# Performance work log

Hardware: AMD Instinct MI355X
Metric: run time of the kernel (lower is better)

Reference implementation:

```python
import jax, jax.numpy as jnp
import numpy as np

# dims
B, S, ENC, MARK = 8, 512, 7, 4
D, I, K, NH = 512, 1024, 4, 8          # embedding_dim, inner=2*D, conv kernel, heads
DH = I // NH                            # 128 per-head dim
BS_BLK = 4                              # qkv_proj_blocksize
NB = I // BS_BLK                        # 256 headwise blocks
L = 4                                   # num_blocks
PRED, COUT = 96, 7
EPS = 1e-6


def ln(x, w):
    mu = jnp.mean(x, -1, keepdims=True)
    var = jnp.var(x, -1, keepdims=True)
    return (x - mu) * jax.lax.rsqrt(var + 1e-5) * w


def causal_conv(x, w, b):
    # x [B,S,I], depthwise causal conv, kernel w [I,K]
    xp = jnp.pad(x, ((0, 0), (K - 1, 0), (0, 0)))
    kern = w.T[:, None, :]  # [K,1,I] for WIO with groups=I
    y = jax.lax.conv_general_dilated(xp, kern, (1,), 'VALID',
                                     dimension_numbers=('NWC', 'WIO', 'NWC'),
                                     feature_group_count=I)
    return y + b


def headwise(t, w):
    # block-diagonal linear (LinearHeadwiseExpand): t [B,S,I], w [NB,BS,BS]
    tb = t.reshape(B, S, NB, BS_BLK)
    return jnp.einsum('bsni,noi->bsno', tb, w).reshape(B, S, I)


def mlstm_parallel(q, k, v, ig, fg):
    # parallel_stabilized_simple: q,k,v [B,NH,S,DH]; ig,fg [B,NH,S]
    lf = jax.nn.log_sigmoid(fg)
    lfc = jnp.concatenate([jnp.zeros_like(lf[..., :1]), jnp.cumsum(lf, -1)], -1)  # [B,NH,S+1]
    m = (lfc[..., :, None] - lfc[..., None, :])[..., 1:, 1:]  # [B,NH,S,S]
    mask = jnp.tril(jnp.ones((S, S), dtype=bool))
    logD = jnp.where(mask, m + ig[..., None, :], -jnp.inf)
    maxD = jnp.max(logD, -1, keepdims=True)
    Dm = jnp.exp(logD - maxD)
    C = jnp.einsum('bnsd,bntd->bnst', q, k) * (DH ** -0.5) * Dm
    n = jnp.maximum(jnp.abs(jnp.sum(C, -1, keepdims=True)), jnp.exp(-maxD))
    return jnp.einsum('bnst,bntd->bnsd', C / (n + EPS), v)


def mh_norm(h, w):
    # per-head layernorm over DH, scale w [I]
    mu = jnp.mean(h, -1, keepdims=True)
    var = jnp.var(h, -1, keepdims=True)
    return (h - mu) * jax.lax.rsqrt(var + 1e-5) * w.reshape(1, NH, 1, DH)


def mlstm_block(x, p):
    lnw, upW, upb, cw, cb, wq, wk, wv, igW, igb, fgW, fgb, onw, skw, dW, db = p
    h = ln(x, lnw)                              # pre-norm
    u = h @ upW + upb                           # [B,S,2I]
    xm, z = jnp.split(u, 2, -1)
    xc = jax.nn.silu(causal_conv(xm, cw, cb))   # conv branch
    q = headwise(xc, wq)
    k = headwise(xc, wk)
    v = headwise(xm, wv)
    g = jnp.concatenate([q, k, v], -1)          # [B,S,3I]
    ig = (g @ igW + igb).transpose(0, 2, 1)     # [B,NH,S]
    fg = (g @ fgW + fgb).transpose(0, 2, 1)
    qh = q.reshape(B, S, NH, DH).transpose(0, 2, 1, 3)
    kh = k.reshape(B, S, NH, DH).transpose(0, 2, 1, 3)
    vh = v.reshape(B, S, NH, DH).transpose(0, 2, 1, 3)
    hh = mlstm_parallel(qh, kh, vh, ig, fg)
    hh = mh_norm(hh, onw).transpose(0, 2, 1, 3).reshape(B, S, I)
    hh = (hh + skw * xc) * jax.nn.silu(z)       # learnable skip + output gate
    return x + hh @ dW + db                     # residual


def setup_inputs() -> dict:
    key = jax.random.key(0)
    ks = jax.random.split(key, 16)
    r = lambda i, shape, s=0.02: jax.random.normal(ks[i], shape, jnp.float32) * s
    return {
        'x_enc': jax.random.normal(ks[0], (B, S, ENC), jnp.float32),
        'x_mark_enc': jax.random.normal(ks[1], (B, S, MARK), jnp.float32),
        'x_dec': jax.random.normal(ks[2], (B, PRED, ENC), jnp.float32),
        'x_mark_dec': jax.random.normal(ks[3], (B, PRED, MARK), jnp.float32),
        'emb_W': r(4, (ENC + MARK, D), 0.1), 'emb_b': jnp.zeros((D,), jnp.float32),
        'blk_ln_w': jnp.ones((L, D), jnp.float32),
        'up_W': r(5, (L, D, 2 * I)), 'up_b': jnp.zeros((L, 2 * I), jnp.float32),
        'conv_w': r(6, (L, I, K), 0.1), 'conv_b': jnp.zeros((L, I), jnp.float32),
        'Wq': r(7, (L, NB, BS_BLK, BS_BLK), 0.3),
        'Wk': r(8, (L, NB, BS_BLK, BS_BLK), 0.3),
        'Wv': r(9, (L, NB, BS_BLK, BS_BLK), 0.3),
        'ig_W': r(10, (L, 3 * I, NH), 0.01), 'ig_b': jnp.full((L, NH), -10.0, jnp.float32),
        'fg_W': r(11, (L, 3 * I, NH), 0.01),
        'fg_b': jnp.tile(jnp.linspace(3.0, 6.0, NH, dtype=jnp.float32)[None], (L, 1)),
        'onorm_w': jnp.ones((L, I), jnp.float32),
        'skip_w': jnp.ones((L, I), jnp.float32),
        'down_W': r(12, (L, I, D)), 'down_b': jnp.zeros((L, D), jnp.float32),
        'post_w': jnp.ones((D,), jnp.float32),
        'head_W': r(13, (D, COUT), 0.05), 'head_b': jnp.zeros((COUT,), jnp.float32),
    }


def reference(x_enc, x_mark_enc, x_dec, x_mark_dec, emb_W, emb_b, blk_ln_w,
              up_W, up_b, conv_w, conv_b, Wq, Wk, Wv, ig_W, ig_b, fg_W, fg_b,
              onorm_w, skip_w, down_W, down_b, post_w, head_W, head_b):
    x = jnp.concatenate([x_enc, x_mark_enc], -1) @ emb_W + emb_b  # [B,S,D]
    params = (blk_ln_w, up_W, up_b, conv_w, conv_b, Wq, Wk, Wv,
              ig_W, ig_b, fg_W, fg_b, onorm_w, skip_w, down_W, down_b)
    def step(c, p):
        return mlstm_block(c, p), None
    x, _ = jax.lax.scan(step, x, params)
    x = ln(x, post_w)                           # post_blocks_norm
    return x[:, -PRED:, :] @ head_W + head_b    # [B,PRED,COUT]
```

## Files before the change

kernel.cpp:

```cpp
#include <hip/hip_runtime.h>
#include <math.h>

static constexpr int kB = 8, kS = 512;
static constexpr int kD = 512, kI = 1024, kNH = 8, kDH = 128;
static constexpr int kL = 4, kPRED = 96, kCOUT = 7;
static constexpr int kM = kB * kS;

typedef __bf16 bf16x8 __attribute__((ext_vector_type(8)));
typedef float f32x4 __attribute__((ext_vector_type(4)));

#define MFMA_BF16(a, b, c) __builtin_amdgcn_mfma_f32_16x16x32_bf16((a), (b), (c), 0, 0, 0)

typedef __attribute__((address_space(1))) const unsigned char* as1cp;
typedef __attribute__((address_space(3))) unsigned char* as3p;
__device__ __forceinline__ void gload16(const void* g, void* l) {
  __builtin_amdgcn_global_load_lds((as1cp)g, (as3p)l, 16, 0, 0);
}

__device__ __forceinline__ unsigned short f2bf(float f) {
  union { float f; unsigned u; } v; v.f = f;
  unsigned r = v.u + 0x7fffu + ((v.u >> 16) & 1u);
  return (unsigned short)(r >> 16);
}
__device__ __forceinline__ float bf2f(unsigned short h) {
  union { unsigned u; float f; } v; v.u = (unsigned)h << 16; return v.f;
}

__global__ __launch_bounds__(256) void embed_ln_kernel(
    const float* __restrict__ xe, const float* __restrict__ xme,
    const float* __restrict__ W, const float* __restrict__ bias,
    const float* __restrict__ lnw,
    float* __restrict__ x, unsigned short* __restrict__ h) {
  int m = blockIdx.x;
  int tid = threadIdx.x;
  __shared__ float f[11];
  if (tid < 7) f[tid] = xe[m * 7 + tid];
  else if (tid < 11) f[tid] = xme[m * 4 + (tid - 7)];
  __syncthreads();
  float v0 = bias[tid], v1 = bias[256 + tid];
#pragma unroll
  for (int e = 0; e < 11; ++e) {
    v0 += f[e] * W[e * kD + tid];
    v1 += f[e] * W[e * kD + 256 + tid];
  }
  x[(size_t)m * kD + tid] = v0;
  x[(size_t)m * kD + 256 + tid] = v1;
  float s1 = v0 + v1, s2 = v0 * v0 + v1 * v1;
#pragma unroll
  for (int o = 1; o < 64; o <<= 1) { s1 += __shfl_xor(s1, o, 64); s2 += __shfl_xor(s2, o, 64); }
  __shared__ float a1[4], a2[4];
  if ((tid & 63) == 0) { a1[tid >> 6] = s1; a2[tid >> 6] = s2; }
  __syncthreads();
  float t1 = a1[0] + a1[1] + a1[2] + a1[3];
  float t2 = a2[0] + a2[1] + a2[2] + a2[3];
  float mu = t1 * (1.f / kD);
  float var = t2 * (1.f / kD) - mu * mu;
  float rs = rsqrtf(var + 1e-5f);
  h[(size_t)m * kD + tid] = f2bf((v0 - mu) * rs * lnw[tid]);
  h[(size_t)m * kD + 256 + tid] = f2bf((v1 - mu) * rs * lnw[256 + tid]);
}

__global__ __launch_bounds__(256) void ln_kernel(
    const float* __restrict__ x, const float* __restrict__ w, unsigned short* __restrict__ h) {
  int m = blockIdx.x, tid = threadIdx.x;
  float v0 = x[(size_t)m * kD + tid];
  float v1 = x[(size_t)m * kD + 256 + tid];
  float s1 = v0 + v1, s2 = v0 * v0 + v1 * v1;
#pragma unroll
  for (int o = 1; o < 64; o <<= 1) { s1 += __shfl_xor(s1, o, 64); s2 += __shfl_xor(s2, o, 64); }
  __shared__ float a1[4], a2[4];
  if ((tid & 63) == 0) { a1[tid >> 6] = s1; a2[tid >> 6] = s2; }
  __syncthreads();
  float t1 = a1[0] + a1[1] + a1[2] + a1[3];
  float t2 = a2[0] + a2[1] + a2[2] + a2[3];
  float mu = t1 * (1.f / kD);
  float var = t2 * (1.f / kD) - mu * mu;
  float rs = rsqrtf(var + 1e-5f);
  h[(size_t)m * kD + tid] = f2bf((v0 - mu) * rs * w[tid]);
  h[(size_t)m * kD + 256 + tid] = f2bf((v1 - mu) * rs * w[256 + tid]);
}

__global__ __launch_bounds__(256) void tpose_all_kernel(
    const float* __restrict__ upW, const float* __restrict__ dnW,
    const float* __restrict__ igW, const float* __restrict__ fgW,
    unsigned short* __restrict__ upWT, unsigned short* __restrict__ dnWT,
    unsigned short* __restrict__ gWT) {
  __shared__ float t[64][65];
  int id = blockIdx.x, tid = threadIdx.x;
  if (id < 1024) {
    int l = id >> 8, rem = id & 255;
    int n0 = (rem >> 3) * 64, k0 = (rem & 7) * 64;
    const float* Wl = upW + (size_t)l * 2048 * 512;
    unsigned short* WTl = upWT + (size_t)l * 2048 * 512;
    for (int idx = tid; idx < 4096; idx += 256) {
      int r = idx >> 6, c = idx & 63;
      t[r][c] = Wl[(size_t)(k0 + r) * 2048 + n0 + c];
    }
    __syncthreads();
    for (int idx = tid; idx < 4096; idx += 256) {
      int r = idx >> 6, c = idx & 63;
      WTl[(size_t)(n0 + r) * 512 + k0 + c] = f2bf(t[c][r]);
    }
  } else if (id < 1536) {
    int tt = id - 1024;
    int l = tt >> 7, rem = tt & 127;
    int n0 = (rem >> 4) * 64, k0 = (rem & 15) * 64;
    const float* Wl = dnW + (size_t)l * 512 * 1024;
    unsigned short* WTl = dnWT + (size_t)l * 512 * 1024;
    for (int idx = tid; idx < 4096; idx += 256) {
      int r = idx >> 6, c = idx & 63;
      t[r][c] = Wl[(size_t)(k0 + r) * 512 + n0 + c];
    }
    __syncthreads();
    for (int idx = tid; idx < 4096; idx += 256) {
      int r = idx >> 6, c = idx & 63;
      WTl[(size_t)(n0 + r) * 1024 + k0 + c] = f2bf(t[c][r]);
    }
  } else {
    int tt = id - 1536;
    int l = tt / 12, kc = tt % 12;
    int k = kc * 256 + tid;
    const float* igl = igW + (size_t)l * 3072 * 8;
    const float* fgl = fgW + (size_t)l * 3072 * 8;
    unsigned short* gl = gWT + (size_t)l * 16 * 3072;
#pragma unroll
    for (int h = 0; h < 8; ++h) {
      gl[(size_t)h * 3072 + k] = f2bf(igl[(size_t)k * 8 + h]);
      gl[(size_t)(8 + h) * 3072 + k] = f2bf(fgl[(size_t)k * 8 + h]);
    }
  }
}

template <int BM, int NBN, int RESID, typename TO>
__global__ __launch_bounds__(256) void gemm_mfma_kernel(
    const unsigned short* __restrict__ A, const unsigned short* __restrict__ BT,
    const float* __restrict__ bias, TO* __restrict__ C, int N, int Kd, int nwg) {
  constexpr int A_ISS = BM / 8;
  constexpr int PER_W = (A_ISS + 16) / 4;
  constexpr int MR = BM / 32;
  __shared__ __align__(16) char As[BM * 128];
  __shared__ __align__(16) char Bs[16384];
  int tid = threadIdx.x, w = tid >> 6, l = tid & 63;
  int lr = l & 15, lg = l >> 4;
  int id = blockIdx.x;
  int q = nwg >> 3, r = nwg & 7;
  int xcd = id & 7, pos = id >> 3;
  int wg = (xcd < r ? xcd * (q + 1) : r * (q + 1) + (xcd - r) * q) + pos;
  int bn = wg % NBN, bm = wg / NBN;
  int wrow = (w >> 1) * (BM / 2), wcol = (w & 1) * 64;
  f32x4 acc[MR][4] = {};
  for (int kt = 0; kt < Kd; kt += 64) {
    __syncthreads();
#pragma unroll
    for (int j = 0; j < PER_W; ++j) {
      int g = w * PER_W + j;
      bool isA = g < A_ISS;
      int ii = isA ? g : g - A_ISS;
      int row = ii * 8 + (l >> 3);
      int chunk = (l & 7) ^ (row & 7);
      const unsigned short* src = isA
          ? A + ((size_t)(bm * BM + row) * Kd + kt) + chunk * 8
          : BT + ((size_t)(bn * 128 + row) * Kd + kt) + chunk * 8;
      char* dst = (isA ? As : Bs) + ii * 1024;
      gload16(src, dst);
    }
    __syncthreads();
#pragma unroll
    for (int kk = 0; kk < 2; ++kk) {
      bf16x8 af[MR], bfr[4];
#pragma unroll
      for (int m = 0; m < MR; ++m) {
        int row = wrow + m * 16 + lr;
        int ch = (kk * 4 + lg) ^ (row & 7);
        af[m] = *(const bf16x8*)(As + row * 128 + ch * 16);
      }
#pragma unroll
      for (int n = 0; n < 4; ++n) {
        int row = wcol + n * 16 + lr;
        int ch = (kk * 4 + lg) ^ (row & 7);
        bfr[n] = *(const bf16x8*)(Bs + row * 128 + ch * 16);
      }
      __builtin_amdgcn_s_setprio(1);
#pragma unroll
      for (int m = 0; m < MR; ++m)
#pragma unroll
        for (int n = 0; n < 4; ++n)
          acc[m][n] = MFMA_BF16(af[m], bfr[n], acc[m][n]);
      __builtin_amdgcn_s_setprio(0);
    }
  }
#pragma unroll
  for (int n = 0; n < 4; ++n) {
    int col = bn * 128 + wcol + n * 16 + lr;
    float bv = bias[col];
#pragma unroll
    for (int m = 0; m < MR; ++m)
#pragma unroll
      for (int i = 0; i < 4; ++i) {
        int row = bm * BM + wrow + m * 16 + lg * 4 + i;
        float v = acc[m][n][i] + bv;
        if constexpr (sizeof(TO) == 2) {
          C[(size_t)row * N + col] = (TO)f2bf(v);
        } else {
          if (RESID) v += C[(size_t)row * N + col];
          C[(size_t)row * N + col] = v;
        }
      }
  }
}

__global__ __launch_bounds__(256) void convhead_kernel(
    const unsigned short* __restrict__ u, const float* __restrict__ cw,
    const float* __restrict__ cb,
    const float* __restrict__ Wq, const float* __restrict__ Wk, const float* __restrict__ Wv,
    unsigned short* __restrict__ xcb, unsigned short* __restrict__ qb,
    unsigned short* __restrict__ kb, unsigned short* __restrict__ vb) {
  int mb = blockIdx.x;
  int b = mb >> 7, sq = (mb & 127) * 4;
  int n = threadIdx.x;
  float xm[7][4];
#pragma unroll
  for (int j = 0; j < 7; ++j) {
    int sp = sq - 3 + j;
    if (sp >= 0) {
      unsigned long long raw = *(const unsigned long long*)&u[((size_t)(b * kS + sp)) * (2 * kI) + n * 4];
#pragma unroll
      for (int i = 0; i < 4; ++i) xm[j][i] = bf2f((unsigned short)(raw >> (i * 16)));
    } else {
#pragma unroll
      for (int i = 0; i < 4; ++i) xm[j][i] = 0.f;
    }
  }
  float4 cb4 = *(const float4*)&cb[n * 4];
  const float* cbp = &cb4.x;
  float cwv[4][4];
#pragma unroll
  for (int i = 0; i < 4; ++i) *(float4*)cwv[i] = *(const float4*)&cw[(n * 4 + i) * 4];
  float wqv[16], wkv[16], wvv[16];
#pragma unroll
  for (int o2 = 0; o2 < 4; ++o2) {
    *(float4*)&wqv[o2 * 4] = *(const float4*)&Wq[n * 16 + o2 * 4];
    *(float4*)&wkv[o2 * 4] = *(const float4*)&Wk[n * 16 + o2 * 4];
    *(float4*)&wvv[o2 * 4] = *(const float4*)&Wv[n * 16 + o2 * 4];
  }
#pragma unroll
  for (int t = 0; t < 4; ++t) {
    int s = sq + t;
    float xc[4];
    unsigned long long xcv = 0;
#pragma unroll
    for (int i = 0; i < 4; ++i) {
      float acc = cbp[i] + xm[t][i] * cwv[i][0] + xm[t + 1][i] * cwv[i][1] +
                  xm[t + 2][i] * cwv[i][2] + xm[t + 3][i] * cwv[i][3];
      xc[i] = acc / (1.f + __expf(-acc));
      xcv |= (unsigned long long)f2bf(xc[i]) << (i * 16);
    }
    *(unsigned long long*)&xcb[((size_t)(b * kS + s)) * kI + n * 4] = xcv;
    unsigned long long qv = 0, kv = 0, vv = 0;
#pragma unroll
    for (int o = 0; o < 4; ++o) {
      float aq = 0, ak = 0, av = 0;
#pragma unroll
      for (int i = 0; i < 4; ++i) {
        aq += xc[i] * wqv[o * 4 + i];
        ak += xc[i] * wkv[o * 4 + i];
        av += xm[t + 3][i] * wvv[o * 4 + i];
      }
      qv |= (unsigned long long)f2bf(aq) << (o * 16);
      kv |= (unsigned long long)f2bf(ak) << (o * 16);
      vv |= (unsigned long long)f2bf(av) << (o * 16);
    }
    size_t base = ((size_t)(b * 8 + (n >> 5)) * kS + s) * kDH + (n & 31) * 4;
    *(unsigned long long*)&qb[base] = qv;
    *(unsigned long long*)&kb[base] = kv;
    *(unsigned long long*)&vb[base] = vv;
  }
}

__global__ __launch_bounds__(256) void prep_kernel(
    const unsigned short* __restrict__ qb, const unsigned short* __restrict__ kb,
    const unsigned short* __restrict__ vb, const unsigned short* __restrict__ gWT,
    float* __restrict__ IGp, float* __restrict__ FGp, unsigned short* __restrict__ vt) {
  __shared__ __align__(16) char smem[16640];
  int id = blockIdx.x;
  int tid = threadIdx.x;
  if (id < 192) {
    int src = id >> 6;
    int blk = id & 63;
    int b = blk >> 3, s0 = (blk & 7) * 64;
    int w = tid >> 6, l = tid & 63;
    int lr = l & 15, lg = l >> 4;
    char* Ts = smem;
    const unsigned short* srcb = (src == 0) ? qb : (src == 1) ? kb : vb;
    f32x4 acc = {};
    for (int kc8 = 0; kc8 < 8; ++kc8) {
      const unsigned short* srcbase = srcb + ((size_t)(b * 8 + kc8) * kS + s0) * kDH;
      __syncthreads();
#pragma unroll
      for (int j = 0; j < 4; ++j) {
        int issue = w * 4 + j;
        int row = issue * 4 + (l >> 4);
        int chunk = (l & 15) ^ (row & 7);
        gload16(srcbase + row * 128 + chunk * 8, Ts + issue * 1024);
      }
      __syncthreads();
#pragma unroll
      for (int kk = 0; kk < 4; ++kk) {
        int arow = w * 16 + lr;
        int ch = (kk * 4 + lg) ^ (arow & 7);
        bf16x8 af = *(const bf16x8*)(Ts + arow * 256 + ch * 16);
        bf16x8 bfv = *(const bf16x8*)(gWT + (size_t)lr * 3072 + (src * 8 + kc8) * 128 + kk * 32 + lg * 8);
        acc = MFMA_BF16(af, bfv, acc);
      }
    }
    float* IGo = IGp + (size_t)src * 64 * kS;
    float* FGo = FGp + (size_t)src * 64 * kS;
#pragma unroll
    for (int i = 0; i < 4; ++i) {
      int s = s0 + w * 16 + lg * 4 + i;
      if (lr < 8) IGo[((size_t)(b * 8) + lr) * kS + s] = acc[i];
      else FGo[((size_t)(b * 8) + lr - 8) * kS + s] = acc[i];
    }
  } else {
    int t = id - 192;
    int bh = t >> 3, s0 = (t & 7) * 64;
    unsigned short (*tt)[130] = (unsigned short(*)[130])smem;
    for (int idx = tid; idx < 64 * 128; idx += 256) {
      int sl = idx >> 7, d = idx & 127;
      tt[sl][d] = vb[((size_t)bh * kS + s0 + sl) * kDH + d];
    }
    __syncthreads();
    for (int idx = tid; idx < 64 * 128; idx += 256) {
      int dl = idx >> 6, sl = idx & 63;
      vt[((size_t)bh * kDH + dl) * kS + s0 + sl] = tt[sl][dl];
    }
  }
}

__global__ __launch_bounds__(512) void mlstm_mfma_kernel(
    const unsigned short* __restrict__ qb, const unsigned short* __restrict__ kb,
    const unsigned short* __restrict__ vt,
    const float* __restrict__ IGp, const float* __restrict__ FGp,
    const float* __restrict__ igb, const float* __restrict__ fgb,
    const unsigned short* __restrict__ u, const unsigned short* __restrict__ xcb,
    const float* __restrict__ onw, const float* __restrict__ skw,
    unsigned short* __restrict__ hhb) {
  int id = blockIdx.x;
  int bh = (id & 7) * 8 + ((id >> 3) & 7);
  int pr = id >> 6;
  int rtA = 7 - pr, rtB = pr;
  int b = bh >> 3, nh = bh & 7;
  int tid = threadIdx.x, w = tid >> 6, l = tid & 63;
  int g = w >> 2, wl = w & 3;
  int rt = (g == 0) ? rtA : rtB;
  int lr = l & 15, lg = l >> 4;
  __shared__ __align__(16) char Ks[2][16384];
  __shared__ __align__(16) char Vs[2][16384];
  __shared__ __align__(16) char Ps[8][2048];
  __shared__ float avs[512], incs[512], pms[512];
  __shared__ float wsum[8], wmax[8];

  const unsigned short* kbh = kb + (size_t)bh * kS * kDH;
  const unsigned short* vbh = vt + (size_t)bh * kDH * kS;

#pragma unroll
  for (int j = 0; j < 2; ++j) {
    int issue = w * 2 + j;
    int row = issue * 4 + (l >> 4);
    int chunk = (l & 15) ^ (row & 7);
    gload16(kbh + row * 128 + chunk * 8, Ks[0] + issue * 1024);
  }
#pragma unroll
  for (int j = 0; j < 2; ++j) {
    int vi = w * 2 + j;
    int row = vi * 8 + (l >> 3);
    int chunk = (l & 7) ^ (row & 7);
    gload16(vbh + (size_t)row * kS + chunk * 8, Vs[0] + vi * 1024);
  }

  {
    int lane = tid & 63, wid2 = tid >> 6;
    const size_t ss = (size_t)64 * kS;
    size_t o = (size_t)bh * kS + tid;
    float igv = IGp[o] + IGp[ss + o] + IGp[2 * ss + o] + igb[nh];
    float fgv = FGp[o] + FGp[ss + o] + FGp[2 * ss + o] + fgb[nh];
    float lf = fminf(fgv, 0.f) - log1pf(__expf(-fabsf(fgv)));
    float x = lf;
#pragma unroll
    for (int off = 1; off < 64; off <<= 1) {
      float v = __shfl_up(x, off, 64);
      if (lane >= off) x += v;
    }
    if (lane == 63) wsum[wid2] = x;
    __syncthreads();
    float base = 0.f;
    for (int i2 = 0; i2 < wid2; ++i2) base += wsum[i2];
    float inct = x + base;
    incs[tid] = inct;
    float av = igv - inct;
    avs[tid] = 0.08838834764831845f * __expf(av);
    float y = av;
#pragma unroll
    for (int off = 1; off < 64; off <<= 1) {
      float v = __shfl_up(y, off, 64);
      if (lane >= off) y = fmaxf(y, v);
    }
    if (lane == 63) wmax[wid2] = y;
    __syncthreads();
    float mb2 = y;
    for (int i2 = 0; i2 < wid2; ++i2) mb2 = fmaxf(mb2, wmax[i2]);
    pms[tid] = mb2;
  }

  bf16x8 qf[4];
  int qrow = rt * 64 + wl * 16 + lr;
  const unsigned short* qrp = qb + ((size_t)bh * kS + qrow) * kDH + lg * 8;
#pragma unroll
  for (int kk = 0; kk < 4; ++kk) qf[kk] = *(const bf16x8*)(qrp + kk * 32);

  __syncthreads();

  float pm_r[4], epm[4];
#pragma unroll
  for (int i = 0; i < 4; ++i) {
    pm_r[i] = pms[rt * 64 + wl * 16 + lg * 4 + i];
    epm[i] = __expf(-pm_r[i]);
  }

  f32x4 oacc[8] = {};
  float rsum[4] = {};

  int cur = 0;
#pragma unroll 1
  for (int ct = 0; ct <= rtA; ++ct) {
    if (ct < rtA) {
      const unsigned short* kbase = kbh + (size_t)(ct + 1) * 64 * kDH;
      const unsigned short* vbase = vbh + (size_t)(ct + 1) * 64;
#pragma unroll
      for (int j = 0; j < 2; ++j) {
        int issue = w * 2 + j;
        int row = issue * 4 + (l >> 4);
        int chunk = (l & 15) ^ (row & 7);
        gload16(kbase + row * 128 + chunk * 8, Ks[cur ^ 1] + issue * 1024);
      }
#pragma unroll
      for (int j = 0; j < 2; ++j) {
        int vi = w * 2 + j;
        int row = vi * 8 + (l >> 3);
        int chunk = (l & 7) ^ (row & 7);
        gload16(vbase + (size_t)row * kS + chunk * 8, Vs[cur ^ 1] + vi * 1024);
      }
    }
    if (ct <= rt) {
      f32x4 sacc[4] = {};
      __builtin_amdgcn_s_setprio(1);
#pragma unroll
      for (int n = 0; n < 4; ++n) {
#pragma unroll
        for (int kk = 0; kk < 4; ++kk) {
          int krow = n * 16 + lr;
          int ch = (kk * 4 + lg) ^ (krow & 7);
          bf16x8 kf = *(const bf16x8*)(Ks[cur] + krow * 256 + ch * 16);
          sacc[n] = MFMA_BF16(qf[kk], kf, sacc[n]);
        }
      }
      __builtin_amdgcn_s_setprio(0);
#pragma unroll
      for (int n = 0; n < 4; ++n) {
        float eav = avs[ct * 64 + n * 16 + lr];
        int cg = ct * 64 + n * 16 + lr;
#pragma unroll
        for (int i = 0; i < 4; ++i) {
          int rg = rt * 64 + wl * 16 + lg * 4 + i;
          float s = 0.f;
          if (ct < rt || cg <= rg)
            s = sacc[n][i] * (eav * epm[i]);
          rsum[i] += s;
          int prow = lg * 4 + i, pcol = n * 16 + lr;
          int byte = prow * 128 + ((((pcol >> 3) ^ (prow & 7))) << 4) + (pcol & 7) * 2;
          *(unsigned short*)(Ps[w] + byte) = f2bf(s);
        }
      }
      __builtin_amdgcn_s_setprio(1);
#pragma unroll
      for (int kk = 0; kk < 2; ++kk) {
        int prow = lr;
        int pch = (kk * 4 + lg) ^ (prow & 7);
        bf16x8 pf = *(const bf16x8*)(Ps[w] + prow * 128 + pch * 16);
#pragma unroll
        for (int nb = 0; nb < 8; ++nb) {
          int vrow = nb * 16 + lr;
          int vch = (kk * 4 + lg) ^ (vrow & 7);
          bf16x8 vf = *(const bf16x8*)(Vs[cur] + vrow * 128 + vch * 16);
          oacc[nb] = MFMA_BF16(pf, vf, oacc[nb]);
        }
      }
      __builtin_amdgcn_s_setprio(0);
    }
    __syncthreads();
    cur ^= 1;
  }

#pragma unroll
  for (int i = 0; i < 4; ++i)
#pragma unroll
    for (int off = 1; off < 16; off <<= 1) rsum[i] += __shfl_xor(rsum[i], off, 16);
  float ninv[4];
#pragma unroll
  for (int i = 0; i < 4; ++i) {
    int rg = rt * 64 + wl * 16 + lg * 4 + i;
    float e0 = __expf(-incs[rg] - pm_r[i]);
    float nn = fmaxf(fabsf(rsum[i]), e0);
    ninv[i] = 1.f / (nn + 1e-6f);
  }
  float val[8][4];
  float s1[4] = {}, s2[4] = {};
#pragma unroll
  for (int nb = 0; nb < 8; ++nb)
#pragma unroll
    for (int i = 0; i < 4; ++i) {
      float v = oacc[nb][i] * ninv[i];
      val[nb][i] = v;
      s1[i] += v; s2[i] += v * v;
    }
#pragma unroll
  for (int i = 0; i < 4; ++i) {
#pragma unroll
    for (int off = 1; off < 16; off <<= 1) {
      s1[i] += __shfl_xor(s1[i], off, 16);
      s2[i] += __shfl_xor(s2[i], off, 16);
    }
  }
#pragma unroll
  for (int i = 0; i < 4; ++i) {
    int rg = rt * 64 + wl * 16 + lg * 4 + i;
    float mu = s1[i] * (1.f / 128.f);
    float var = s2[i] * (1.f / 128.f) - mu * mu;
    float rstd = rsqrtf(var + 1e-5f);
    size_t rowbase = (size_t)(b * kS + rg);
#pragma unroll
    for (int nb = 0; nb < 8; ++nb) {
      int c = nh * kDH + nb * 16 + lr;
      float nv = (val[nb][i] - mu) * rstd * onw[c];
      float z = bf2f(u[rowbase * (2 * kI) + kI + c]);
      float sz = z / (1.f + __expf(-z));
      float xcv = bf2f(xcb[rowbase * kI + c]);
      hhb[rowbase * kI + c] = f2bf((nv + skw[c] * xcv) * sz);
    }
  }
}

__global__ __launch_bounds__(256) void head_kernel(
    const float* __restrict__ x, const float* __restrict__ pw,
    const float* __restrict__ hW, const float* __restrict__ hb, float* __restrict__ out) {
  int row = blockIdx.x;
  int b = row / kPRED, p = row % kPRED;
  int m = b * kS + (kS - kPRED) + p;
  int tid = threadIdx.x;
  float v0 = x[(size_t)m * kD + tid];
  float v1 = x[(size_t)m * kD + 256 + tid];
  float s1 = v0 + v1, s2 = v0 * v0 + v1 * v1;
#pragma unroll
  for (int o = 1; o < 64; o <<= 1) { s1 += __shfl_xor(s1, o, 64); s2 += __shfl_xor(s2, o, 64); }
  __shared__ float a1[4], a2[4];
  if ((tid & 63) == 0) { a1[tid >> 6] = s1; a2[tid >> 6] = s2; }
  __syncthreads();
  float t1 = a1[0] + a1[1] + a1[2] + a1[3];
  float t2 = a2[0] + a2[1] + a2[2] + a2[3];
  float mu = t1 * (1.f / kD);
  float var = t2 * (1.f / kD) - mu * mu;
  float rs = rsqrtf(var + 1e-5f);
  __shared__ float buf[512];
  buf[tid] = (v0 - mu) * rs * pw[tid];
  buf[256 + tid] = (v1 - mu) * rs * pw[256 + tid];
  __syncthreads();
  float acc[7] = {};
  for (int kk = tid; kk < 512; kk += 256) {
    float g = buf[kk];
#pragma unroll
    for (int n = 0; n < 7; ++n) acc[n] += g * hW[kk * 7 + n];
  }
  __shared__ float red[256 * 9];
#pragma unroll
  for (int n = 0; n < 7; ++n) red[tid * 9 + n] = acc[n];
  __syncthreads();
  for (int off = 128; off >= 1; off >>= 1) {
    if (tid < off) {
#pragma unroll
      for (int n = 0; n < 7; ++n) red[tid * 9 + n] += red[(tid + off) * 9 + n];
    }
    __syncthreads();
  }
  if (tid < 7) out[(size_t)row * 7 + tid] = red[tid] + hb[tid];
}

extern "C" void kernel_launch(void* const* d_in, const int* in_sizes, int n_in,
                              void* d_out, int out_size, void* d_ws, size_t ws_size,
                              hipStream_t stream) {
  const float* x_enc    = (const float*)d_in[0];
  const float* x_mark   = (const float*)d_in[1];
  const float* emb_W    = (const float*)d_in[4];
  const float* emb_b    = (const float*)d_in[5];
  const float* blk_ln_w = (const float*)d_in[6];
  const float* up_W     = (const float*)d_in[7];
  const float* up_b     = (const float*)d_in[8];
  const float* conv_w   = (const float*)d_in[9];
  const float* conv_b   = (const float*)d_in[10];
  const float* Wq       = (const float*)d_in[11];
  const float* Wk       = (const float*)d_in[12];
  const float* Wv       = (const float*)d_in[13];
  const float* ig_W     = (const float*)d_in[14];
  const float* ig_b     = (const float*)d_in[15];
  const float* fg_W     = (const float*)d_in[16];
  const float* fg_b     = (const float*)d_in[17];
  const float* onorm_w  = (const float*)d_in[18];
  const float* skip_w   = (const float*)d_in[19];
  const float* down_W   = (const float*)d_in[20];
  const float* down_b   = (const float*)d_in[21];
  const float* post_w   = (const float*)d_in[22];
  const float* head_W   = (const float*)d_in[23];
  const float* head_b   = (const float*)d_in[24];
  float* out = (float*)d_out;

  char* ws = (char*)d_ws;
  float* X  = (float*)ws;                     ws += (size_t)kM * kD * 4;
  unsigned short* U    = (unsigned short*)ws; ws += (size_t)kM * 2 * kI * 2;
  unsigned short* XCb  = (unsigned short*)ws; ws += (size_t)kM * kI * 2;
  unsigned short* Hb   = (unsigned short*)ws; ws += (size_t)kM * kD * 2;
  unsigned short* HHb  = (unsigned short*)ws; ws += (size_t)kM * kI * 2;
  unsigned short* qb   = (unsigned short*)ws; ws += (size_t)kM * kI * 2;
  unsigned short* kbuf = (unsigned short*)ws; ws += (size_t)kM * kI * 2;
  unsigned short* vb   = (unsigned short*)ws; ws += (size_t)kM * kI * 2;
  unsigned short* vt   = (unsigned short*)ws; ws += (size_t)kM * kI * 2;
  unsigned short* upWT = (unsigned short*)ws; ws += (size_t)kL * 2 * kI * kD * 2;
  unsigned short* dnWT = (unsigned short*)ws; ws += (size_t)kL * kD * kI * 2;
  unsigned short* gWT  = (unsigned short*)ws; ws += (size_t)kL * 16 * 3072 * 2;
  float* IGp = (float*)ws; ws += (size_t)3 * 64 * kS * 4;
  float* FGp = (float*)ws; ws += (size_t)3 * 64 * kS * 4;

  embed_ln_kernel<<<kM, 256, 0, stream>>>(x_enc, x_mark, emb_W, emb_b, blk_ln_w, X, Hb);
  tpose_all_kernel<<<1584, 256, 0, stream>>>(up_W, down_W, ig_W, fg_W, upWT, dnWT, gWT);

  for (int l = 0; l < kL; ++l) {
    const float* lnw  = blk_ln_w + (size_t)l * kD;
    const float* upbl = up_b + (size_t)l * 2 * kI;
    const float* cwl  = conv_w + (size_t)l * kI * 4;
    const float* cbl  = conv_b + (size_t)l * kI;
    const float* wql  = Wq + (size_t)l * 256 * 16;
    const float* wkl  = Wk + (size_t)l * 256 * 16;
    const float* wvl  = Wv + (size_t)l * 256 * 16;
    const float* igbl = ig_b + (size_t)l * kNH;
    const float* fgbl = fg_b + (size_t)l * kNH;
    const float* onwl = onorm_w + (size_t)l * kI;
    const float* skwl = skip_w + (size_t)l * kI;
    const float* dbl  = down_b + (size_t)l * kD;
    const unsigned short* upWTl = upWT + (size_t)l * 2 * kI * kD;
    const unsigned short* dnWTl = dnWT + (size_t)l * kD * kI;
    const unsigned short* gWTl  = gWT + (size_t)l * 16 * 3072;

    if (l > 0) ln_kernel<<<kM, 256, 0, stream>>>(X, lnw, Hb);
    gemm_mfma_kernel<128, 16, 0, unsigned short><<<512, 256, 0, stream>>>(
        Hb, upWTl, upbl, U, 2 * kI, kD, 512);
    convhead_kernel<<<1024, 256, 0, stream>>>(U, cwl, cbl, wql, wkl, wvl, XCb, qb, kbuf, vb);
    prep_kernel<<<704, 256, 0, stream>>>(qb, kbuf, vb, gWTl, IGp, FGp, vt);
    mlstm_mfma_kernel<<<256, 512, 0, stream>>>(
        qb, kbuf, vt, IGp, FGp, igbl, fgbl, U, XCb, onwl, skwl, HHb);
    gemm_mfma_kernel<64, 4, 1, float><<<256, 256, 0, stream>>>(
        HHb, dnWTl, dbl, X, kD, kI, 256);
  }

  head_kernel<<<kB * kPRED, 256, 0, stream>>>(X, post_w, head_W, head_b, out);
}
```

Baseline: 388.4 us.

## Fold block LayerNorm into up-projection GEMM epilogue via row stats and colsums

Removes the per-layer LayerNorm kernel. The down-projection GEMM epilogue now writes a bf16 copy of the residual stream plus partial per-row sum and sum-of-squares. The up GEMM multiplies raw bf16 x by weights pre-scaled with the LN weight, then applies mean and rstd correction using precomputed weight column sums. The embedding, transpose and colsum setup are merged into one init kernel. This saves a launch and a memory pass per layer. The cost is extra epilogue work, and the numerics differ because normalization happens after bf16 quantization of the un-centered x, with possible cancellation error.

```diff
diff --git a/kernel.cpp b/kernel.cpp
--- a/kernel.cpp
+++ b/kernel.cpp
@@ -26,71 +26,52 @@
   union { unsigned u; float f; } v; v.u = (unsigned)h << 16; return v.f;
 }
 
-__global__ __launch_bounds__(256) void embed_ln_kernel(
+__global__ __launch_bounds__(256) void init_kernel(
     const float* __restrict__ xe, const float* __restrict__ xme,
-    const float* __restrict__ W, const float* __restrict__ bias,
-    const float* __restrict__ lnw,
-    float* __restrict__ x, unsigned short* __restrict__ h) {
-  int m = blockIdx.x;
-  int tid = threadIdx.x;
-  __shared__ float f[11];
-  if (tid < 7) f[tid] = xe[m * 7 + tid];
-  else if (tid < 11) f[tid] = xme[m * 4 + (tid - 7)];
-  __syncthreads();
-  float v0 = bias[tid], v1 = bias[256 + tid];
-#pragma unroll
-  for (int e = 0; e < 11; ++e) {
-    v0 += f[e] * W[e * kD + tid];
-    v1 += f[e] * W[e * kD + 256 + tid];
-  }
-  x[(size_t)m * kD + tid] = v0;
-  x[(size_t)m * kD + 256 + tid] = v1;
-  float s1 = v0 + v1, s2 = v0 * v0 + v1 * v1;
-#pragma unroll
-  for (int o = 1; o < 64; o <<= 1) { s1 += __shfl_xor(s1, o, 64); s2 += __shfl_xor(s2, o, 64); }
-  __shared__ float a1[4], a2[4];
-  if ((tid & 63) == 0) { a1[tid >> 6] = s1; a2[tid >> 6] = s2; }
-  __syncthreads();
-  float t1 = a1[0] + a1[1] + a1[2] + a1[3];
-  float t2 = a2[0] + a2[1] + a2[2] + a2[3];
-  float mu = t1 * (1.f / kD);
-  float var = t2 * (1.f / kD) - mu * mu;
-  float rs = rsqrtf(var + 1e-5f);
-  h[(size_t)m * kD + tid] = f2bf((v0 - mu) * rs * lnw[tid]);
-  h[(size_t)m * kD + 256 + tid] = f2bf((v1 - mu) * rs * lnw[256 + tid]);
-}
-
-__global__ __launch_bounds__(256) void ln_kernel(
-    const float* __restrict__ x, const float* __restrict__ w, unsigned short* __restrict__ h) {
-  int m = blockIdx.x, tid = threadIdx.x;
-  float v0 = x[(size_t)m * kD + tid];
-  float v1 = x[(size_t)m * kD + 256 + tid];
-  float s1 = v0 + v1, s2 = v0 * v0 + v1 * v1;
-#pragma unroll
-  for (int o = 1; o < 64; o <<= 1) { s1 += __shfl_xor(s1, o, 64); s2 += __shfl_xor(s2, o, 64); }
-  __shared__ float a1[4], a2[4];
-  if ((tid & 63) == 0) { a1[tid >> 6] = s1; a2[tid >> 6] = s2; }
-  __syncthreads();
-  float t1 = a1[0] + a1[1] + a1[2] + a1[3];
-  float t2 = a2[0] + a2[1] + a2[2] + a2[3];
-  float mu = t1 * (1.f / kD);
-  float var = t2 * (1.f / kD) - mu * mu;
-  float rs = rsqrtf(var + 1e-5f);
-  h[(size_t)m * kD + tid] = f2bf((v0 - mu) * rs * w[tid]);
-  h[(size_t)m * kD + 256 + tid] = f2bf((v1 - mu) * rs * w[256 + tid]);
-}
-
-__global__ __launch_bounds__(256) void tpose_all_kernel(
+    const float* __restrict__ embW, const float* __restrict__ embb,
+    const float* __restrict__ lnw_all,
     const float* __restrict__ upW, const float* __restrict__ dnW,
     const float* __restrict__ igW, const float* __restrict__ fgW,
+    float* __restrict__ x, unsigned short* __restrict__ xb,
+    float* __restrict__ st1, float* __restrict__ st2,
     unsigned short* __restrict__ upWT, unsigned short* __restrict__ dnWT,
-    unsigned short* __restrict__ gWT) {
+    unsigned short* __restrict__ gWT, float* __restrict__ colsum) {
   __shared__ float t[64][65];
+  __shared__ float f[11], a1[4], a2[4];
   int id = blockIdx.x, tid = threadIdx.x;
-  if (id < 1024) {
-    int l = id >> 8, rem = id & 255;
+  if (id < 4096) {
+    int m = id;
+    if (tid < 7) f[tid] = xe[m * 7 + tid];
+    else if (tid < 11) f[tid] = xme[m * 4 + (tid - 7)];
+    __syncthreads();
+    float v0 = embb[tid], v1 = embb[256 + tid];
+#pragma unroll
+    for (int e = 0; e < 11; ++e) {
+      v0 += f[e] * embW[e * kD + tid];
+      v1 += f[e] * embW[e * kD + 256 + tid];
+    }
+    x[(size_t)m * kD + tid] = v0;
+    x[(size_t)m * kD + 256 + tid] = v1;
+    xb[(size_t)m * kD + tid] = f2bf(v0);
+    xb[(size_t)m * kD + 256 + tid] = f2bf(v1);
+    float s1 = v0 + v1, s2 = v0 * v0 + v1 * v1;
+#pragma unroll
+    for (int o = 1; o < 64; o <<= 1) { s1 += __shfl_xor(s1, o, 64); s2 += __shfl_xor(s2, o, 64); }
+    if ((tid & 63) == 0) { a1[tid >> 6] = s1; a2[tid >> 6] = s2; }
+    __syncthreads();
+    if (tid == 0) {
+      st1[m] = a1[0] + a1[1] + a1[2] + a1[3];
+      st2[m] = a2[0] + a2[1] + a2[2] + a2[3];
+    } else if (tid < 4) {
+      st1[tid * 4096 + m] = 0.f;
+      st2[tid * 4096 + m] = 0.f;
+    }
+  } else if (id < 5120) {
+    int tt = id - 4096;
+    int l = tt >> 8, rem = tt & 255;
     int n0 = (rem >> 3) * 64, k0 = (rem & 7) * 64;
     const float* Wl = upW + (size_t)l * 2048 * 512;
+    const float* lnw = lnw_all + (size_t)l * kD;
     unsigned short* WTl = upWT + (size_t)l * 2048 * 512;
     for (int idx = tid; idx < 4096; idx += 256) {
       int r = idx >> 6, c = idx & 63;
@@ -99,10 +80,10 @@
     __syncthreads();
     for (int idx = tid; idx < 4096; idx += 256) {
       int r = idx >> 6, c = idx & 63;
-      WTl[(size_t)(n0 + r) * 512 + k0 + c] = f2bf(t[c][r]);
-    }
-  } else if (id < 1536) {
-    int tt = id - 1024;
+      WTl[(size_t)(n0 + r) * 512 + k0 + c] = f2bf(lnw[k0 + c] * t[c][r]);
+    }
+  } else if (id < 5632) {
+    int tt = id - 5120;
     int l = tt >> 7, rem = tt & 127;
     int n0 = (rem >> 4) * 64, k0 = (rem & 15) * 64;
     const float* Wl = dnW + (size_t)l * 512 * 1024;
@@ -116,8 +97,8 @@
       int r = idx >> 6, c = idx & 63;
       WTl[(size_t)(n0 + r) * 1024 + k0 + c] = f2bf(t[c][r]);
     }
-  } else {
-    int tt = id - 1536;
+  } else if (id < 5680) {
+    int tt = id - 5632;
     int l = tt / 12, kc = tt % 12;
     int k = kc * 256 + tid;
     const float* igl = igW + (size_t)l * 3072 * 8;
@@ -128,16 +109,25 @@
       gl[(size_t)h * 3072 + k] = f2bf(igl[(size_t)k * 8 + h]);
       gl[(size_t)(8 + h) * 3072 + k] = f2bf(fgl[(size_t)k * 8 + h]);
     }
-  }
-}
-
-template <int BM, int NBN, int RESID, typename TO>
-__global__ __launch_bounds__(256) void gemm_mfma_kernel(
+  } else {
+    int tt = id - 5680;
+    int l = tt >> 3, n = (tt & 7) * 256 + tid;
+    const float* Wl = upW + (size_t)l * 2048 * 512;
+    const float* lnw = lnw_all + (size_t)l * kD;
+    float cs = 0.f;
+    for (int k = 0; k < 512; ++k)
+      cs += bf2f(f2bf(lnw[k] * Wl[(size_t)k * 2048 + n]));
+    colsum[(size_t)l * 2048 + n] = cs;
+  }
+}
+
+__global__ __launch_bounds__(256) void gemm_up_kernel(
     const unsigned short* __restrict__ A, const unsigned short* __restrict__ BT,
-    const float* __restrict__ bias, TO* __restrict__ C, int N, int Kd, int nwg) {
-  constexpr int A_ISS = BM / 8;
-  constexpr int PER_W = (A_ISS + 16) / 4;
-  constexpr int MR = BM / 32;
+    const float* __restrict__ bias, const float* __restrict__ colsum,
+    const float* __restrict__ st1, const float* __restrict__ st2,
+    unsigned short* __restrict__ C, int nwg) {
+  constexpr int BM = 128, NBN = 16, Kd = 512, N = 2048;
+  constexpr int A_ISS = BM / 8, PER_W = (A_ISS + 16) / 4, MR = BM / 32;
   __shared__ __align__(16) char As[BM * 128];
   __shared__ __align__(16) char Bs[16384];
   int tid = threadIdx.x, w = tid >> 6, l = tid & 63;
@@ -189,23 +179,140 @@
       __builtin_amdgcn_s_setprio(0);
     }
   }
+  float mu_r[MR][4], rs_r[MR][4];
+#pragma unroll
+  for (int m = 0; m < MR; ++m)
+#pragma unroll
+    for (int i = 0; i < 4; ++i) {
+      int row = bm * BM + wrow + m * 16 + lg * 4 + i;
+      float s1 = st1[row] + st1[4096 + row] + st1[8192 + row] + st1[12288 + row];
+      float s2 = st2[row] + st2[4096 + row] + st2[8192 + row] + st2[12288 + row];
+      float mu = s1 * (1.f / 512.f);
+      float var = s2 * (1.f / 512.f) - mu * mu;
+      mu_r[m][i] = mu;
+      rs_r[m][i] = rsqrtf(var + 1e-5f);
+    }
 #pragma unroll
   for (int n = 0; n < 4; ++n) {
     int col = bn * 128 + wcol + n * 16 + lr;
     float bv = bias[col];
+    float cs = colsum[col];
 #pragma unroll
     for (int m = 0; m < MR; ++m)
 #pragma unroll
       for (int i = 0; i < 4; ++i) {
         int row = bm * BM + wrow + m * 16 + lg * 4 + i;
-        float v = acc[m][n][i] + bv;
-        if constexpr (sizeof(TO) == 2) {
-          C[(size_t)row * N + col] = (TO)f2bf(v);
-        } else {
-          if (RESID) v += C[(size_t)row * N + col];
-          C[(size_t)row * N + col] = v;
-        }
-      }
+        float v = rs_r[m][i] * (acc[m][n][i] - mu_r[m][i] * cs) + bv;
+        C[(size_t)row * N + col] = f2bf(v);
+      }
+  }
+}
+
+__global__ __launch_bounds__(256) void gemm_dn_kernel(
+    const unsigned short* __restrict__ A, const unsigned short* __restrict__ BT,
+    const float* __restrict__ bias, float* __restrict__ X,
+    unsigned short* __restrict__ Xb, float* __restrict__ st1, float* __restrict__ st2,
+    int nwg) {
+  constexpr int BM = 64, NBN = 4, Kd = 1024, N = 512;
+  constexpr int A_ISS = BM / 8, PER_W = (A_ISS + 16) / 4, MR = BM / 32;
+  __shared__ __align__(16) char As[BM * 128];
+  __shared__ __align__(16) char Bs[16384];
+  __shared__ float sst[4][32][2];
+  int tid = threadIdx.x, w = tid >> 6, l = tid & 63;
+  int lr = l & 15, lg = l >> 4;
+  int id = blockIdx.x;
+  int q = nwg >> 3, r = nwg & 7;
+  int xcd = id & 7, pos = id >> 3;
+  int wg = (xcd < r ? xcd * (q + 1) : r * (q + 1) + (xcd - r) * q) + pos;
+  int bn = wg % NBN, bm = wg / NBN;
+  int wrow = (w >> 1) * (BM / 2), wcol = (w & 1) * 64;
+  f32x4 acc[MR][4] = {};
+  for (int kt = 0; kt < Kd; kt += 64) {
+    __syncthreads();
+#pragma unroll
+    for (int j = 0; j < PER_W; ++j) {
+      int g = w * PER_W + j;
+      bool isA = g < A_ISS;
+      int ii = isA ? g : g - A_ISS;
+      int row = ii * 8 + (l >> 3);
+      int chunk = (l & 7) ^ (row & 7);
+      const unsigned short* src = isA
+          ? A + ((size_t)(bm * BM + row) * Kd + kt) + chunk * 8
+          : BT + ((size_t)(bn * 128 + row) * Kd + kt) + chunk * 8;
+      char* dst = (isA ? As : Bs) + ii * 1024;
+      gload16(src, dst);
+    }
+    __syncthreads();
+#pragma unroll
+    for (int kk = 0; kk < 2; ++kk) {
+      bf16x8 af[MR], bfr[4];
+#pragma unroll
+      for (int m = 0; m < MR; ++m) {
+        int row = wrow + m * 16 + lr;
+        int ch = (kk * 4 + lg) ^ (row & 7);
+        af[m] = *(const bf16x8*)(As + row * 128 + ch * 16);
+      }
+#pragma unroll
+      for (int n = 0; n < 4; ++n) {
+        int row = wcol + n * 16 + lr;
+        int ch = (kk * 4 + lg) ^ (row & 7);
+        bfr[n] = *(const bf16x8*)(Bs + row * 128 + ch * 16);
+      }
+      __builtin_amdgcn_s_setprio(1);
+#pragma unroll
+      for (int m = 0; m < MR; ++m)
+#pragma unroll
+        for (int n = 0; n < 4; ++n)
+          acc[m][n] = MFMA_BF16(af[m], bfr[n], acc[m][n]);
+      __builtin_amdgcn_s_setprio(0);
+    }
+  }
+  float ps1[MR][4] = {}, ps2[MR][4] = {};
+#pragma unroll
+  for (int n = 0; n < 4; ++n) {
+    int col = bn * 128 + wcol + n * 16 + lr;
+    float bv = bias[col];
+#pragma unroll
+    for (int m = 0; m < MR; ++m)
+#pragma unroll
+      for (int i = 0; i < 4; ++i) {
+        int row = bm * BM + wrow + m * 16 + lg * 4 + i;
+        float v = acc[m][n][i] + bv + X[(size_t)row * N + col];
+        X[(size_t)row * N + col] = v;
+        Xb[(size_t)row * N + col] = f2bf(v);
+        ps1[m][i] += v;
+        ps2[m][i] += v * v;
+      }
+  }
+#pragma unroll
+  for (int m = 0; m < MR; ++m)
+#pragma unroll
+    for (int i = 0; i < 4; ++i) {
+#pragma unroll
+      for (int off = 1; off < 16; off <<= 1) {
+        ps1[m][i] += __shfl_xor(ps1[m][i], off, 16);
+        ps2[m][i] += __shfl_xor(ps2[m][i], off, 16);
+      }
+    }
+  if (lr == 0) {
+#pragma unroll
+    for (int m = 0; m < MR; ++m)
+#pragma unroll
+      for (int i = 0; i < 4; ++i) {
+        int lrow = m * 16 + lg * 4 + i;
+        sst[w][lrow][0] = ps1[m][i];
+        sst[w][lrow][1] = ps2[m][i];
+      }
+  }
+  __syncthreads();
+  if (tid < 64) {
+    int lrow = tid & 31, half = tid >> 5;
+    int wA = half * 2, wB = half * 2 + 1;
+    float s1 = sst[wA][lrow][0] + sst[wB][lrow][0];
+    float s2 = sst[wA][lrow][1] + sst[wB][lrow][1];
+    int grow = bm * BM + half * 32 + lrow;
+    st1[(size_t)bn * 4096 + grow] = s1;
+    st2[(size_t)bn * 4096 + grow] = s2;
   }
 }
 
@@ -624,9 +731,9 @@
 
   char* ws = (char*)d_ws;
   float* X  = (float*)ws;                     ws += (size_t)kM * kD * 4;
+  unsigned short* Xb   = (unsigned short*)ws; ws += (size_t)kM * kD * 2;
   unsigned short* U    = (unsigned short*)ws; ws += (size_t)kM * 2 * kI * 2;
   unsigned short* XCb  = (unsigned short*)ws; ws += (size_t)kM * kI * 2;
-  unsigned short* Hb   = (unsigned short*)ws; ws += (size_t)kM * kD * 2;
   unsigned short* HHb  = (unsigned short*)ws; ws += (size_t)kM * kI * 2;
   unsigned short* qb   = (unsigned short*)ws; ws += (size_t)kM * kI * 2;
   unsigned short* kbuf = (unsigned short*)ws; ws += (size_t)kM * kI * 2;
@@ -637,12 +744,15 @@
   unsigned short* gWT  = (unsigned short*)ws; ws += (size_t)kL * 16 * 3072 * 2;
   float* IGp = (float*)ws; ws += (size_t)3 * 64 * kS * 4;
   float* FGp = (float*)ws; ws += (size_t)3 * 64 * kS * 4;
-
-  embed_ln_kernel<<<kM, 256, 0, stream>>>(x_enc, x_mark, emb_W, emb_b, blk_ln_w, X, Hb);
-  tpose_all_kernel<<<1584, 256, 0, stream>>>(up_W, down_W, ig_W, fg_W, upWT, dnWT, gWT);
+  float* ST1 = (float*)ws; ws += (size_t)4 * kM * 4;
+  float* ST2 = (float*)ws; ws += (size_t)4 * kM * 4;
+  float* CSUM = (float*)ws; ws += (size_t)kL * 2 * kI * 4;
+
+  init_kernel<<<5712, 256, 0, stream>>>(
+      x_enc, x_mark, emb_W, emb_b, blk_ln_w, up_W, down_W, ig_W, fg_W,
+      X, Xb, ST1, ST2, upWT, dnWT, gWT, CSUM);
 
   for (int l = 0; l < kL; ++l) {
-    const float* lnw  = blk_ln_w + (size_t)l * kD;
     const float* upbl = up_b + (size_t)l * 2 * kI;
     const float* cwl  = conv_w + (size_t)l * kI * 4;
     const float* cbl  = conv_b + (size_t)l * kI;
@@ -657,16 +767,14 @@
     const unsigned short* upWTl = upWT + (size_t)l * 2 * kI * kD;
     const unsigned short* dnWTl = dnWT + (size_t)l * kD * kI;
     const unsigned short* gWTl  = gWT + (size_t)l * 16 * 3072;
-
-    if (l > 0) ln_kernel<<<kM, 256, 0, stream>>>(X, lnw, Hb);
-    gemm_mfma_kernel<128, 16, 0, unsigned short><<<512, 256, 0, stream>>>(
-        Hb, upWTl, upbl, U, 2 * kI, kD, 512);
+    const float* csuml = CSUM + (size_t)l * 2 * kI;
+
+    gemm_up_kernel<<<512, 256, 0, stream>>>(Xb, upWTl, upbl, csuml, ST1, ST2, U, 512);
     convhead_kernel<<<1024, 256, 0, stream>>>(U, cwl, cbl, wql, wkl, wvl, XCb, qb, kbuf, vb);
     prep_kernel<<<704, 256, 0, stream>>>(qb, kbuf, vb, gWTl, IGp, FGp, vt);
     mlstm_mfma_kernel<<<256, 512, 0, stream>>>(
         qb, kbuf, vt, IGp, FGp, igbl, fgbl, U, XCb, onwl, skwl, HHb);
-    gemm_mfma_kernel<64, 4, 1, float><<<256, 256, 0, stream>>>(
-        HHb, dnWTl, dbl, X, kD, kI, 256);
+    gemm_dn_kernel<<<256, 256, 0, stream>>>(HHb, dnWTl, dbl, X, Xb, ST1, ST2, 256);
   }
 
   head_kernel<<<kB * kPRED, 256, 0, stream>>>(X, post_w, head_W, head_b, out);
```

New measurement: 383.3 us. About the same (-1.3%).
